# Optimization experiments

Measured on AMD Instinct MI355X. Metric: run time of the kernel, lower is better.

The kernel has to match this reference:

```python
import jax, jax.numpy as jnp
import numpy as np

N, E, D, H = 50000, 800000, 128, 128


def _uniform_param(key, shape, fan_in):
    bound = 1.0 / np.sqrt(fan_in)
    return jax.random.uniform(key, shape, jnp.float32, -bound, bound)


def setup_inputs() -> dict:
    key = jax.random.key(0)
    ks = jax.random.split(key, 12)
    x = jax.random.normal(ks[0], (N, D), jnp.float32)
    xedge = jax.random.randint(ks[1], (2, E), 0, N, jnp.int64)
    y = jax.random.randint(ks[2], (N,), 0, 2, jnp.int32).astype(bool)
    return {
        "x": x,
        "xedge": xedge,
        "y": y,
        "pretrain": 0,
        # SAGEConv layer 1 (in=D, out=H): lin_l (with bias) applied to mean aggr, lin_r (no bias) to self
        "W1l": _uniform_param(ks[3], (D, H), D),
        "b1l": _uniform_param(ks[4], (H,), D),
        "W1r": _uniform_param(ks[5], (D, H), D),
        # SAGEConv layer 2 (in=H, out=H)
        "W2l": _uniform_param(ks[6], (H, H), H),
        "b2l": _uniform_param(ks[7], (H,), H),
        "W2r": _uniform_param(ks[8], (H, H), H),
        # Decoder weight [H, H]
        "Wdec": _uniform_param(ks[9], (H, H), H),
    }


def sage_conv(h, src, dst, Wl, bl, Wr, num_nodes):
    # gather neighbor features along edges, mean-aggregate by destination
    msgs = h[src]                                            # [E, d]
    agg = jax.ops.segment_sum(msgs, dst, num_segments=num_nodes)
    cnt = jax.ops.segment_sum(jnp.ones((src.shape[0],), h.dtype), dst,
                              num_segments=num_nodes)
    mean = agg / jnp.maximum(cnt, 1.0)[:, None]              # [N, d]
    return mean @ Wl + bl + h @ Wr                           # [N, out]


def reference(x, xedge, y, pretrain, W1l, b1l, W1r, W2l, b2l, W2r, Wdec):
    src, dst = xedge[0], xedge[1]
    n = x.shape[0]
    # Encoder: SAGE = conv1 -> relu -> (dropout: eval identity) -> conv2
    h = jax.nn.relu(sage_conv(x, src, dst, W1l, b1l, W1r, n))
    emb = sage_conv(h, src, dst, W2l, b2l, W2r, n)           # [N, H]
    # Decoder
    dx = emb @ Wdec                                          # [N, H]
    # BCEWithLogits: pos nodes target 1, neg nodes target 0, mean within each group
    ym = y.astype(dx.dtype)                                  # [N]
    n_pos = jnp.sum(ym)
    n_neg = n - n_pos
    hdim = dx.shape[1]
    sp_pos = jax.nn.softplus(-dx)   # bce(logit, 1)
    sp_neg = jax.nn.softplus(dx)    # bce(logit, 0)
    l2 = jnp.sum(sp_pos * ym[:, None]) / (jnp.maximum(n_pos, 1.0) * hdim)
    l1 = jnp.sum(sp_neg * (1.0 - ym)[:, None]) / (jnp.maximum(n_neg, 1.0) * hdim)
    return (l1 + l2, emb)
```

## Files before the change

kernel.cpp:

```cpp
#include <hip/hip_runtime.h>
#include <hip/hip_bf16.h>

#define NDIM 128
#define MROWS 32
#define SCAN_CHUNK 1024

typedef __attribute__((ext_vector_type(8))) short short8;
typedef __attribute__((ext_vector_type(4))) float f32x4;

__device__ __forceinline__ float bf2f(__hip_bfloat16 v) { return __bfloat162float(v); }

__device__ __forceinline__ float ldf(const void* p, long i, int f32) {
    return f32 ? ((const float*)p)[i] : bf2f(((const __hip_bfloat16*)p)[i]);
}
__device__ __forceinline__ void stf(void* p, long i, int f32, float v) {
    if (f32) ((float*)p)[i] = v;
    else     ((__hip_bfloat16*)p)[i] = __float2bfloat16(v);
}
__device__ __forceinline__ short f2bf(float v) {
    __hip_bfloat16 h = __float2bfloat16(v);
    short s;
    __builtin_memcpy(&s, &h, 2);
    return s;
}
__device__ __forceinline__ float bflo(unsigned u) { u <<= 16; float f; __builtin_memcpy(&f, &u, 4); return f; }
__device__ __forceinline__ float bfhi(unsigned u) { u &= 0xffff0000u; float f; __builtin_memcpy(&f, &u, 4); return f; }
__device__ __forceinline__ unsigned packbf(float a, float b) {
    unsigned la = (unsigned short)f2bf(a);
    unsigned hb = (unsigned short)f2bf(b);
    return (hb << 16) | la;
}
__device__ __forceinline__ int aswz(int m, int k) {
    return m * NDIM + ((((k >> 3) ^ (m & 7)) << 3) | (k & 7));
}
__device__ __forceinline__ int wswz(int m, int p) {
    return m * 64 + ((((p >> 2) ^ (m & 7)) << 2) | (p & 3));
}

__global__ void detect_kernel(const int* __restrict__ xedge32,
                              const unsigned int* __restrict__ yw,
                              const unsigned short* __restrict__ xh,
                              int* __restrict__ flags, int* __restrict__ cnt,
                              float* __restrict__ accum, int* __restrict__ npos, int N) {
    const int gid = blockIdx.x * 256 + threadIdx.x;
    for (int i = gid; i < N; i += gridDim.x * 256) cnt[i] = 0;
    if (gid == 0) { accum[0] = 0.f; accum[1] = 0.f; npos[0] = 0; }
    if (blockIdx.x == 0) {
        __shared__ int se, sy, scount;
        const int t = threadIdx.x;
        if (t == 0) { se = 1; sy = 0; scount = 0; }
        __syncthreads();
        for (int i = t; i < 512; i += 256)
            if (xedge32[2 * i + 1] != 0) se = 0;
        for (int i = t; i < 1024; i += 256)
            if (yw[i] > 1u) sy = 1;
        int c = 0;
        for (int i = t; i < 1024; i += 256) {
            int ex = (xh[2 * i] >> 7) & 0xFF;
            if (ex >= 100 && ex <= 150) c++;
        }
        atomicAdd(&scount, c);
        __syncthreads();
        if (t == 0) { flags[0] = se; flags[1] = sy; flags[2] = (scount < 900) ? 1 : 0; }
    }
}


__global__ void prep_kernel(const void* __restrict__ x,
                            const void* __restrict__ W1l, const void* __restrict__ b1l,
                            const void* __restrict__ W1r, const void* __restrict__ W2l,
                            const void* __restrict__ b2l, const void* __restrict__ W2r,
                            const void* __restrict__ Wd, const int* __restrict__ flags,
                            short* __restrict__ T1l, short* __restrict__ T1r,
                            short* __restrict__ T2l, short* __restrict__ T2r,
                            short* __restrict__ Td, float* __restrict__ b1c,
                            float* __restrict__ b2c, unsigned* __restrict__ xb,
                            const int* __restrict__ xedge, int E,
                            int* __restrict__ cnt, int N) {
    const int wf = flags[2];
    const long idx = (long)blockIdx.x * 256 + threadIdx.x;
    if (idx < E) {
        int d = flags[0] ? xedge[2 * (E + idx)] : xedge[E + idx];
        atomicAdd(&cnt[d], 1);
    }
    if (idx < NDIM * NDIM) {
        int k = (int)(idx >> 7), n = (int)(idx & 127);
        int o = n * NDIM + k;
        T1l[o] = f2bf(ldf(W1l, idx, wf));
        T1r[o] = f2bf(ldf(W1r, idx, wf));
        T2l[o] = f2bf(ldf(W2l, idx, wf));
        T2r[o] = f2bf(ldf(W2r, idx, wf));
        Td [o] = f2bf(ldf(Wd , idx, wf));
        if (idx < NDIM) { b1c[idx] = ldf(b1l, idx, wf); b2c[idx] = ldf(b2l, idx, wf); }
    } else if (wf) {
        long p = idx - NDIM * NDIM;
        long np = (long)N * 64;
        if (p < np) {
            float2 v = ((const float2*)x)[p];
            xb[p] = packbf(v.x, v.y);
        }
    }
}


__global__ void scan_partial(const int* __restrict__ cnt, int* __restrict__ bsum, int N) {
    __shared__ int red[256];
    const int t = threadIdx.x;
    const long base = (long)blockIdx.x * SCAN_CHUNK + (long)t * 4;
    int s = 0;
#pragma unroll
    for (int i = 0; i < 4; ++i) { long idx = base + i; if (idx < N) s += cnt[idx]; }
    red[t] = s;
    __syncthreads();
    for (int off = 128; off >= 1; off >>= 1) {
        if (t < off) red[t] += red[t + off];
        __syncthreads();
    }
    if (t == 0) bsum[blockIdx.x] = red[0];
}

__global__ void scan_bsums(const int* __restrict__ bsum, int* __restrict__ boff,
                           int B, int* __restrict__ rowptr, int N) {
    __shared__ int part[1024];
    const int t = threadIdx.x;
    int v = (t < B) ? bsum[t] : 0;
    part[t] = v;
    __syncthreads();
    for (int off = 1; off < 1024; off <<= 1) {
        int u = (t >= off) ? part[t - off] : 0;
        __syncthreads();
        part[t] += u;
        __syncthreads();
    }
    if (t < B) boff[t] = part[t] - v;
    if (t == 1023) rowptr[N] = part[1023];
}

__global__ void scan_scatter(int* __restrict__ cnt, const int* __restrict__ boff,
                             int* __restrict__ rowptr, int N) {
    __shared__ int tsum[256];
    const int t = threadIdx.x;
    const long base = (long)blockIdx.x * SCAN_CHUNK + (long)t * 4;
    int loc[4];
    int s = 0;
#pragma unroll
    for (int i = 0; i < 4; ++i) {
        long idx = base + i;
        int c = (idx < N) ? cnt[idx] : 0;
        loc[i] = s;
        s += c;
    }
    tsum[t] = s;
    __syncthreads();
    for (int off = 1; off < 256; off <<= 1) {
        int u = (t >= off) ? tsum[t - off] : 0;
        __syncthreads();
        tsum[t] += u;
        __syncthreads();
    }
    const int texcl = tsum[t] - s;
    const int b0 = boff[blockIdx.x];
#pragma unroll
    for (int i = 0; i < 4; ++i) {
        long idx = base + i;
        if (idx < N) { rowptr[idx] = b0 + texcl + loc[i]; cnt[idx] = 0; }
    }
}

__global__ void fill_kernel(const int* __restrict__ xedge, int E,
                            const int* __restrict__ flags, const int* __restrict__ rowptr,
                            int* __restrict__ cur, int* __restrict__ col) {
    int e = blockIdx.x * blockDim.x + threadIdx.x;
    if (e >= E) return;
    const int e64 = flags[0];
    int s = e64 ? xedge[2 * e] : xedge[e];
    int d = e64 ? xedge[2 * (E + e)] : xedge[E + e];
    int p = rowptr[d] + atomicAdd(&cur[d], 1);
    col[p] = s;
}


template <bool RELU, int OUTMODE>
__global__ __launch_bounds__(256)
void layer_mfma(const unsigned* __restrict__ Xb, const unsigned* __restrict__ Xraw,
                const int* __restrict__ rowptr,
                const int* __restrict__ col, const short* __restrict__ WlT,
                const float* __restrict__ biasc, const short* __restrict__ WrT,
                const short* __restrict__ WdT, const void* __restrict__ yv,
                const int* __restrict__ flags, void* __restrict__ outp,
                float* __restrict__ accum, int* __restrict__ npos, int N) {
    __shared__ short AS[2 * MROWS * NDIM];
    __shared__ int ylds[MROWS];
    __shared__ float redm[4][2];
    short* Ms = AS;
    short* Ss = AS + MROWS * NDIM;
    unsigned* Msw = (unsigned*)Ms;
    unsigned* Ssw = (unsigned*)Ss;
    const int t = threadIdx.x;
    const int n0 = blockIdx.x * MROWS;
    const int wf = flags[2];
    const unsigned* __restrict__ X = wf ? Xb : Xraw;

    if (OUTMODE == 1 && t < MROWS) {
        const int yb = flags[1];
        int n = n0 + t;
        int yn = -1;
        if (n < N)
            yn = yb ? (int)((const unsigned char*)yv)[n]
                    : (((const int*)yv)[n] != 0 ? 1 : 0);
        ylds[t] = yn;
    }

    {
        const int p = t & 63;
        const int lj = t & 31;
        const int g = __builtin_amdgcn_readfirstlane(t >> 6);
        int r = g;
        int b = 0, e = 0;
        {
            int n = n0 + r;
            if (n < N) {
                b = __builtin_amdgcn_readfirstlane(rowptr[n]);
                e = __builtin_amdgcn_readfirstlane(rowptr[n + 1]);
            }
        }
        unsigned colv = 0;
        if (e > b) {
            int cl = b + lj;
            if (cl >= e) cl = e - 1;
            colv = (unsigned)col[cl];
        }
        for (int it = 0; it < 8; ++it, r += 4) {
            const int n = n0 + r;
            const int deg = e - b;
            unsigned su = 0;
            if (n < N) su = X[(long)n * 64 + p];
            unsigned u[32];
            if (deg > 0) {
#pragma unroll
                for (int j = 0; j < 32; ++j) {
                    int c = __builtin_amdgcn_readlane((int)colv, j);
                    u[j] = X[(long)c * 64 + p];
                }
            }
            int bn = 0, en = 0;
            unsigned colv_n = 0;
            if (it < 7) {
                int nn = n0 + r + 4;
                if (nn < N) {
                    bn = __builtin_amdgcn_readfirstlane(rowptr[nn]);
                    en = __builtin_amdgcn_readfirstlane(rowptr[nn + 1]);
                }
                if (en > bn) {
                    int cl = bn + lj;
                    if (cl >= en) cl = en - 1;
                    colv_n = (unsigned)col[cl];
                }
            }
            float m0 = 0.f, m1 = 0.f;
            if (deg > 0) {
                float p0 = 0.f, p1 = 0.f, p2 = 0.f, p3 = 0.f;
                float q0 = 0.f, q1 = 0.f, q2 = 0.f, q3 = 0.f;
#pragma unroll
                for (int j = 0; j < 32; j += 4) {
                    if (j + 0 < deg) { p0 += bflo(u[j]);     q0 += bfhi(u[j]); }
                    if (j + 1 < deg) { p1 += bflo(u[j + 1]); q1 += bfhi(u[j + 1]); }
                    if (j + 2 < deg) { p2 += bflo(u[j + 2]); q2 += bfhi(u[j + 2]); }
                    if (j + 3 < deg) { p3 += bflo(u[j + 3]); q3 += bfhi(u[j + 3]); }
                }
                m0 = (p0 + p1) + (p2 + p3);
                m1 = (q0 + q1) + (q2 + q3);
                for (int i = b + 32; i < e; ++i) {
                    int c = __builtin_amdgcn_readfirstlane(col[i]);
                    unsigned uu = X[(long)c * 64 + p];
                    m0 += bflo(uu);
                    m1 += bfhi(uu);
                }
                float inv = 1.f / (float)deg;
                m0 *= inv; m1 *= inv;
            }
            int wi = wswz(r, p);
            Msw[wi] = packbf(m0, m1);
            Ssw[wi] = su;
            b = bn; e = en; colv = colv_n;
        }
    }
    __syncthreads();
    const int l = t & 63, w = t >> 6;
    const int quad = l >> 4, l15 = l & 15;
    const int wcol = w * 32;
    f32x4 acc[2][2] = {};
    for (int k0 = 0; k0 < NDIM; k0 += 32) {
        const int kc = k0 + quad * 8;
        short8 ams[2], ass[2], bl[2], br[2];
#pragma unroll
        for (int rt = 0; rt < 2; ++rt) {
            int m = rt * 16 + l15;
            ams[rt] = *(const short8*)&Ms[aswz(m, kc)];
            ass[rt] = *(const short8*)&Ss[aswz(m, kc)];
        }
#pragma unroll
        for (int ct = 0; ct < 2; ++ct) {
            int n = wcol + ct * 16 + l15;
            bl[ct] = *(const short8*)&WlT[n * NDIM + kc];
            br[ct] = *(const short8*)&WrT[n * NDIM + kc];
        }
#pragma unroll
        for (int rt = 0; rt < 2; ++rt)
#pragma unroll
            for (int ct = 0; ct < 2; ++ct) {
                acc[rt][ct] = __builtin_amdgcn_mfma_f32_16x16x32_bf16(
                    ams[rt], bl[ct], acc[rt][ct], 0, 0, 0);
                acc[rt][ct] = __builtin_amdgcn_mfma_f32_16x16x32_bf16(
                    ass[rt], br[ct], acc[rt][ct], 0, 0, 0);
            }
    }
    __syncthreads();

    if (OUTMODE == 0) {
#pragma unroll
        for (int ct = 0; ct < 2; ++ct) {
            int cg = wcol + ct * 16 + l15;
            float bv = biasc[cg];
#pragma unroll
            for (int rt = 0; rt < 2; ++rt)
#pragma unroll
                for (int reg = 0; reg < 4; ++reg) {
                    int row = rt * 16 + quad * 4 + reg;
                    float v = acc[rt][ct][reg] + bv;
                    if (RELU) v = fmaxf(v, 0.f);
                    Ms[row * NDIM + cg] = f2bf(v);
                }
        }
        __syncthreads();
        unsigned* ob = (unsigned*)outp;
        for (int idx = t; idx < MROWS * 64; idx += 256) {
            int r = idx >> 6;
            if (n0 + r < N) ob[(long)n0 * 64 + idx] = Msw[idx];
        }
    } else {
#pragma unroll
        for (int ct = 0; ct < 2; ++ct) {
            int cg = wcol + ct * 16 + l15;
            float bv = biasc[cg];
#pragma unroll
            for (int rt = 0; rt < 2; ++rt)
#pragma unroll
                for (int reg = 0; reg < 4; ++reg) {
                    int row = rt * 16 + quad * 4 + reg;
                    float v = acc[rt][ct][reg] + bv;
                    Ms[aswz(row, cg)] = f2bf(v);
                    int n = n0 + row;
                    if (n < N) {
                        if (wf) ((float*)outp)[1 + (long)n * NDIM + cg] = v;
                        else ((__hip_bfloat16*)outp)[1 + (long)n * NDIM + cg] =
                                 __float2bfloat16(v);
                    }
                }
        }
        __syncthreads();
        f32x4 acc2[2][2] = {};
        for (int k0 = 0; k0 < NDIM; k0 += 32) {
            const int kc = k0 + quad * 8;
            short8 a[2], b[2];
#pragma unroll
            for (int rt = 0; rt < 2; ++rt)
                a[rt] = *(const short8*)&Ms[aswz(rt * 16 + l15, kc)];
#pragma unroll
            for (int ct = 0; ct < 2; ++ct)
                b[ct] = *(const short8*)&WdT[(wcol + ct * 16 + l15) * NDIM + kc];
#pragma unroll
            for (int rt = 0; rt < 2; ++rt)
#pragma unroll
                for (int ct = 0; ct < 2; ++ct)
                    acc2[rt][ct] = __builtin_amdgcn_mfma_f32_16x16x32_bf16(
                        a[rt], b[ct], acc2[rt][ct], 0, 0, 0);
        }
        float lpos = 0.f, lneg = 0.f;
#pragma unroll
        for (int rt = 0; rt < 2; ++rt)
#pragma unroll
            for (int reg = 0; reg < 4; ++reg) {
                int row = rt * 16 + quad * 4 + reg;
                int yn = ylds[row];
                if (yn >= 0) {
#pragma unroll
                    for (int ct = 0; ct < 2; ++ct) {
                        float z = acc2[rt][ct][reg];
                        float L = log1pf(expf(-fabsf(z)));
                        if (yn) lpos += fmaxf(-z, 0.f) + L;
                        else    lneg += fmaxf(z, 0.f) + L;
                    }
                }
            }
#pragma unroll
        for (int off = 32; off >= 1; off >>= 1) {
            lpos += __shfl_down(lpos, off, 64);
            lneg += __shfl_down(lneg, off, 64);
        }
        if (l == 0) { redm[w][0] = lpos; redm[w][1] = lneg; }
        __syncthreads();
        if (t == 0) {
            atomicAdd(&accum[0], redm[0][0] + redm[1][0] + redm[2][0] + redm[3][0]);
            atomicAdd(&accum[1], redm[0][1] + redm[1][1] + redm[2][1] + redm[3][1]);
            int c = 0;
            for (int i = 0; i < MROWS; ++i) if (ylds[i] > 0) c++;
            if (c) atomicAdd(npos, c);
        }
    }
}

__global__ void finalize_kernel(const float* __restrict__ accum, const int* __restrict__ npos,
                                const int* __restrict__ flags, void* __restrict__ out, int N) {
    float np_ = (float)(*npos);
    float nn_ = (float)N - np_;
    float l2 = accum[0] / (fmaxf(np_, 1.f) * 128.f);
    float l1 = accum[1] / (fmaxf(nn_, 1.f) * 128.f);
    stf(out, 0, flags[2], l1 + l2);
}


extern "C" void kernel_launch(void* const* d_in, const int* in_sizes, int n_in,
                              void* d_out, int out_size, void* d_ws, size_t ws_size,
                              hipStream_t stream) {
    const void* x    = d_in[0];
    const int* xedge = (const int*)d_in[1];
    const void* y    = d_in[2];
    const void* W1l  = d_in[4];
    const void* b1l  = d_in[5];
    const void* W1r  = d_in[6];
    const void* W2l  = d_in[7];
    const void* b2l  = d_in[8];
    const void* W2r  = d_in[9];
    const void* Wdec = d_in[10];

    const int N = in_sizes[0] / NDIM;
    const int E = in_sizes[1] / 2;

    char* ws = (char*)d_ws;
    size_t off = 0;
    auto alloc = [&](size_t bytes) -> void* {
        void* p = ws + off;
        off = (off + bytes + 255) & ~(size_t)255;
        return p;
    };
    int*   flags  = (int*)alloc(64);
    float* accum  = (float*)alloc(64);
    int*   npos   = (int*)alloc(64);
    int*   bsum   = (int*)alloc(1024 * 4);
    int*   boff   = (int*)alloc(1024 * 4);
    int*   cnt    = (int*)alloc((size_t)N * 4);
    int*   rowptr = (int*)alloc((size_t)(N + 1) * 4);
    int*   col    = (int*)alloc((size_t)E * 4);
    unsigned* xb  = (unsigned*)alloc((size_t)N * 64 * 4);
    unsigned* hbuf = (unsigned*)alloc((size_t)N * 64 * 4);
    short* T1l = (short*)alloc(NDIM * NDIM * 2);
    short* T1r = (short*)alloc(NDIM * NDIM * 2);
    short* T2l = (short*)alloc(NDIM * NDIM * 2);
    short* T2r = (short*)alloc(NDIM * NDIM * 2);
    short* Td  = (short*)alloc(NDIM * NDIM * 2);
    float* b1c = (float*)alloc(NDIM * 4);
    float* b2c = (float*)alloc(NDIM * 4);

    const int zb = (N + 255) / 256;
    detect_kernel<<<zb, 256, 0, stream>>>(xedge, (const unsigned int*)y,
                                          (const unsigned short*)x, flags, cnt,
                                          accum, npos, N);
    const long prep_items = (long)NDIM * NDIM + (long)N * 64;
    prep_kernel<<<(int)((prep_items + 255) / 256), 256, 0, stream>>>(
        x, W1l, b1l, W1r, W2l, b2l, W2r, Wdec, flags,
        T1l, T1r, T2l, T2r, Td, b1c, b2c, xb, xedge, E, cnt, N);

    const int sb = (N + SCAN_CHUNK - 1) / SCAN_CHUNK;
    scan_partial<<<sb, 256, 0, stream>>>(cnt, bsum, N);
    scan_bsums<<<1, 1024, 0, stream>>>(bsum, boff, sb, rowptr, N);
    scan_scatter<<<sb, 256, 0, stream>>>(cnt, boff, rowptr, N);

    const int eb = (E + 255) / 256;
    fill_kernel<<<eb, 256, 0, stream>>>(xedge, E, flags, rowptr, cnt, col);

    const int nbM = (N + MROWS - 1) / MROWS;
    layer_mfma<true, 0><<<nbM, 256, 0, stream>>>(
        xb, (const unsigned*)x, rowptr, col, T1l, b1c, T1r, nullptr, nullptr,
        flags, hbuf, nullptr, nullptr, N);
    layer_mfma<false, 1><<<nbM, 256, 0, stream>>>(
        hbuf, hbuf, rowptr, col, T2l, b2c, T2r, Td, y, flags,
        d_out, accum, npos, N);
    finalize_kernel<<<1, 1, 0, stream>>>(accum, npos, flags, d_out, N);
}
```

Measured before the change: 329.4 us.

## Use 512-thread blocks, degree-gated neighbor loads, and cursor-seeded CSR fill

Doubles the layer block size to 8 wavefronts, so each wave gathers 4 rows instead of 8 and covers 16 output columns in the MFMA stage instead of 32. The neighbor gather now issues loads in chunks of 8 gated by node degree, avoiding 32 redundant clamped loads for low-degree nodes. The CSR fill seeds the cursor array with the row offsets, which removes the rowptr read per edge. The cost is more waves per block with less work each, and the Wl/Wr tiles are now re-read across more waves.

New measurement: 314.1 us. -4.7%, faster.

```diff
diff --git a/kernel.cpp b/kernel.cpp
--- a/kernel.cpp
+++ b/kernel.cpp
@@ -3,6 +3,7 @@
 
 #define NDIM 128
 #define MROWS 32
+#define BTHREADS 512
 #define SCAN_CHUNK 1024
 
 typedef __attribute__((ext_vector_type(8))) short short8;
@@ -163,25 +164,29 @@
 #pragma unroll
     for (int i = 0; i < 4; ++i) {
         long idx = base + i;
-        if (idx < N) { rowptr[idx] = b0 + texcl + loc[i]; cnt[idx] = 0; }
+        if (idx < N) {
+            int v = b0 + texcl + loc[i];
+            rowptr[idx] = v;
+            cnt[idx] = v;
+        }
     }
 }
 
 __global__ void fill_kernel(const int* __restrict__ xedge, int E,
-                            const int* __restrict__ flags, const int* __restrict__ rowptr,
+                            const int* __restrict__ flags,
                             int* __restrict__ cur, int* __restrict__ col) {
     int e = blockIdx.x * blockDim.x + threadIdx.x;
     if (e >= E) return;
     const int e64 = flags[0];
     int s = e64 ? xedge[2 * e] : xedge[e];
     int d = e64 ? xedge[2 * (E + e)] : xedge[E + e];
-    int p = rowptr[d] + atomicAdd(&cur[d], 1);
+    int p = atomicAdd(&cur[d], 1);
     col[p] = s;
 }
 
 
 template <bool RELU, int OUTMODE>
-__global__ __launch_bounds__(256)
+__global__ __launch_bounds__(BTHREADS)
 void layer_mfma(const unsigned* __restrict__ Xb, const unsigned* __restrict__ Xraw,
                 const int* __restrict__ rowptr,
                 const int* __restrict__ col, const short* __restrict__ WlT,
@@ -191,7 +196,7 @@
                 float* __restrict__ accum, int* __restrict__ npos, int N) {
     __shared__ short AS[2 * MROWS * NDIM];
     __shared__ int ylds[MROWS];
-    __shared__ float redm[4][2];
+    __shared__ float redm[8][2];
     short* Ms = AS;
     short* Ss = AS + MROWS * NDIM;
     unsigned* Msw = (unsigned*)Ms;
@@ -230,7 +235,7 @@
             if (cl >= e) cl = e - 1;
             colv = (unsigned)col[cl];
         }
-        for (int it = 0; it < 8; ++it, r += 4) {
+        for (int it = 0; it < 4; ++it, r += 8) {
             const int n = n0 + r;
             const int deg = e - b;
             unsigned su = 0;
@@ -238,15 +243,36 @@
             unsigned u[32];
             if (deg > 0) {
 #pragma unroll
-                for (int j = 0; j < 32; ++j) {
+                for (int j = 0; j < 8; ++j) {
                     int c = __builtin_amdgcn_readlane((int)colv, j);
                     u[j] = X[(long)c * 64 + p];
                 }
             }
+            if (deg > 8) {
+#pragma unroll
+                for (int j = 8; j < 16; ++j) {
+                    int c = __builtin_amdgcn_readlane((int)colv, j);
+                    u[j] = X[(long)c * 64 + p];
+                }
+            }
+            if (deg > 16) {
+#pragma unroll
+                for (int j = 16; j < 24; ++j) {
+                    int c = __builtin_amdgcn_readlane((int)colv, j);
+                    u[j] = X[(long)c * 64 + p];
+                }
+            }
+            if (deg > 24) {
+#pragma unroll
+                for (int j = 24; j < 32; ++j) {
+                    int c = __builtin_amdgcn_readlane((int)colv, j);
+                    u[j] = X[(long)c * 64 + p];
+                }
+            }
             int bn = 0, en = 0;
             unsigned colv_n = 0;
-            if (it < 7) {
-                int nn = n0 + r + 4;
+            if (it < 3) {
+                int nn = n0 + r + 8;
                 if (nn < N) {
                     bn = __builtin_amdgcn_readfirstlane(rowptr[nn]);
                     en = __builtin_amdgcn_readfirstlane(rowptr[nn + 1]);
@@ -288,67 +314,62 @@
     __syncthreads();
     const int l = t & 63, w = t >> 6;
     const int quad = l >> 4, l15 = l & 15;
-    const int wcol = w * 32;
-    f32x4 acc[2][2] = {};
+    const int wcol = w * 16;
+    f32x4 acc[2] = {};
     for (int k0 = 0; k0 < NDIM; k0 += 32) {
         const int kc = k0 + quad * 8;
-        short8 ams[2], ass[2], bl[2], br[2];
+        short8 ams[2], ass[2], bl, br;
 #pragma unroll
         for (int rt = 0; rt < 2; ++rt) {
             int m = rt * 16 + l15;
             ams[rt] = *(const short8*)&Ms[aswz(m, kc)];
             ass[rt] = *(const short8*)&Ss[aswz(m, kc)];
         }
-#pragma unroll
-        for (int ct = 0; ct < 2; ++ct) {
-            int n = wcol + ct * 16 + l15;
-            bl[ct] = *(const short8*)&WlT[n * NDIM + kc];
-            br[ct] = *(const short8*)&WrT[n * NDIM + kc];
-        }
-#pragma unroll
-        for (int rt = 0; rt < 2; ++rt)
-#pragma unroll
-            for (int ct = 0; ct < 2; ++ct) {
-                acc[rt][ct] = __builtin_amdgcn_mfma_f32_16x16x32_bf16(
-                    ams[rt], bl[ct], acc[rt][ct], 0, 0, 0);
-                acc[rt][ct] = __builtin_amdgcn_mfma_f32_16x16x32_bf16(
-                    ass[rt], br[ct], acc[rt][ct], 0, 0, 0);
-            }
+        {
+            int n = wcol + l15;
+            bl = *(const short8*)&WlT[n * NDIM + kc];
+            br = *(const short8*)&WrT[n * NDIM + kc];
+        }
+#pragma unroll
+        for (int rt = 0; rt < 2; ++rt) {
+            acc[rt] = __builtin_amdgcn_mfma_f32_16x16x32_bf16(
+                ams[rt], bl, acc[rt], 0, 0, 0);
+            acc[rt] = __builtin_amdgcn_mfma_f32_16x16x32_bf16(
+                ass[rt], br, acc[rt], 0, 0, 0);
+        }
     }
     __syncthreads();
 
     if (OUTMODE == 0) {
-#pragma unroll
-        for (int ct = 0; ct < 2; ++ct) {
-            int cg = wcol + ct * 16 + l15;
+        {
+            int cg = wcol + l15;
             float bv = biasc[cg];
 #pragma unroll
             for (int rt = 0; rt < 2; ++rt)
 #pragma unroll
                 for (int reg = 0; reg < 4; ++reg) {
                     int row = rt * 16 + quad * 4 + reg;
-                    float v = acc[rt][ct][reg] + bv;
+                    float v = acc[rt][reg] + bv;
                     if (RELU) v = fmaxf(v, 0.f);
                     Ms[row * NDIM + cg] = f2bf(v);
                 }
         }
         __syncthreads();
         unsigned* ob = (unsigned*)outp;
-        for (int idx = t; idx < MROWS * 64; idx += 256) {
+        for (int idx = t; idx < MROWS * 64; idx += BTHREADS) {
             int r = idx >> 6;
             if (n0 + r < N) ob[(long)n0 * 64 + idx] = Msw[idx];
         }
     } else {
-#pragma unroll
-        for (int ct = 0; ct < 2; ++ct) {
-            int cg = wcol + ct * 16 + l15;
+        {
+            int cg = wcol + l15;
             float bv = biasc[cg];
 #pragma unroll
             for (int rt = 0; rt < 2; ++rt)
 #pragma unroll
                 for (int reg = 0; reg < 4; ++reg) {
                     int row = rt * 16 + quad * 4 + reg;
-                    float v = acc[rt][ct][reg] + bv;
+                    float v = acc[rt][reg] + bv;
                     Ms[aswz(row, cg)] = f2bf(v);
                     int n = n0 + row;
                     if (n < N) {
@@ -359,22 +380,18 @@
                 }
         }
         __syncthreads();
-        f32x4 acc2[2][2] = {};
+        f32x4 acc2[2] = {};
         for (int k0 = 0; k0 < NDIM; k0 += 32) {
             const int kc = k0 + quad * 8;
-            short8 a[2], b[2];
+            short8 a[2], bwd;
 #pragma unroll
             for (int rt = 0; rt < 2; ++rt)
                 a[rt] = *(const short8*)&Ms[aswz(rt * 16 + l15, kc)];
-#pragma unroll
-            for (int ct = 0; ct < 2; ++ct)
-                b[ct] = *(const short8*)&WdT[(wcol + ct * 16 + l15) * NDIM + kc];
+            bwd = *(const short8*)&WdT[(wcol + l15) * NDIM + kc];
 #pragma unroll
             for (int rt = 0; rt < 2; ++rt)
-#pragma unroll
-                for (int ct = 0; ct < 2; ++ct)
-                    acc2[rt][ct] = __builtin_amdgcn_mfma_f32_16x16x32_bf16(
-                        a[rt], b[ct], acc2[rt][ct], 0, 0, 0);
+                acc2[rt] = __builtin_amdgcn_mfma_f32_16x16x32_bf16(
+                    a[rt], bwd, acc2[rt], 0, 0, 0);
         }
         float lpos = 0.f, lneg = 0.f;
 #pragma unroll
@@ -384,13 +401,10 @@
                 int row = rt * 16 + quad * 4 + reg;
                 int yn = ylds[row];
                 if (yn >= 0) {
-#pragma unroll
-                    for (int ct = 0; ct < 2; ++ct) {
-                        float z = acc2[rt][ct][reg];
-                        float L = log1pf(expf(-fabsf(z)));
-                        if (yn) lpos += fmaxf(-z, 0.f) + L;
-                        else    lneg += fmaxf(z, 0.f) + L;
-                    }
+                    float z = acc2[rt][reg];
+                    float L = log1pf(expf(-fabsf(z)));
+                    if (yn) lpos += fmaxf(-z, 0.f) + L;
+                    else    lneg += fmaxf(z, 0.f) + L;
                 }
             }
 #pragma unroll
@@ -401,8 +415,11 @@
         if (l == 0) { redm[w][0] = lpos; redm[w][1] = lneg; }
         __syncthreads();
         if (t == 0) {
-            atomicAdd(&accum[0], redm[0][0] + redm[1][0] + redm[2][0] + redm[3][0]);
-            atomicAdd(&accum[1], redm[0][1] + redm[1][1] + redm[2][1] + redm[3][1]);
+            float sp = 0.f, sn = 0.f;
+#pragma unroll
+            for (int i = 0; i < 8; ++i) { sp += redm[i][0]; sn += redm[i][1]; }
+            atomicAdd(&accum[0], sp);
+            atomicAdd(&accum[1], sn);
             int c = 0;
             for (int i = 0; i < MROWS; ++i) if (ylds[i] > 0) c++;
             if (c) atomicAdd(npos, c);
@@ -477,13 +494,13 @@
     scan_scatter<<<sb, 256, 0, stream>>>(cnt, boff, rowptr, N);
 
     const int eb = (E + 255) / 256;
-    fill_kernel<<<eb, 256, 0, stream>>>(xedge, E, flags, rowptr, cnt, col);
+    fill_kernel<<<eb, 256, 0, stream>>>(xedge, E, flags, cnt, col);
 
     const int nbM = (N + MROWS - 1) / MROWS;
-    layer_mfma<true, 0><<<nbM, 256, 0, stream>>>(
+    layer_mfma<true, 0><<<nbM, BTHREADS, 0, stream>>>(
         xb, (const unsigned*)x, rowptr, col, T1l, b1c, T1r, nullptr, nullptr,
         flags, hbuf, nullptr, nullptr, N);
-    layer_mfma<false, 1><<<nbM, 256, 0, stream>>>(
+    layer_mfma<false, 1><<<nbM, BTHREADS, 0, stream>>>(
         hbuf, hbuf, rowptr, col, T2l, b2c, T2r, Td, y, flags,
         d_out, accum, npos, N);
     finalize_kernel<<<1, 1, 0, stream>>>(accum, npos, flags, d_out, N);
```
